# Performance work log

Hardware: AMD Instinct MI355X
Metric: run time of the kernel (lower is better)

## Reference

```python
import jax, jax.numpy as jnp
import numpy as np

N_NODES = 100000
N_EDGES = 1250000
N_GRAPHS = 512
HIDDEN = 64
F_IN = 3
N_CLASSES = 5


def setup_inputs() -> dict:
    key = jax.random.key(0)
    ks = jax.random.split(key, 8)
    x = jax.random.normal(ks[0], (N_NODES, F_IN), dtype=jnp.float32)
    edge_index = jax.random.randint(ks[1], (2, N_EDGES), 0, N_NODES, dtype=jnp.int64)
    batch = jnp.sort(jax.random.randint(ks[2], (N_NODES,), 0, N_GRAPHS, dtype=jnp.int64))
    def glorot(k, shape):
        lim = (6.0 / (shape[0] + shape[1])) ** 0.5
        return jax.random.uniform(k, shape, jnp.float32, -lim, lim)
    return {
        "x": x,
        "edge_index": edge_index,
        "batch": batch,
        "W1": glorot(ks[3], (F_IN, HIDDEN)),
        "b1": jnp.zeros((HIDDEN,), jnp.float32),
        "W2": glorot(ks[4], (HIDDEN, HIDDEN)),
        "b2": jnp.zeros((HIDDEN,), jnp.float32),
        "Wl": glorot(ks[5], (HIDDEN, N_CLASSES)),
        "bl": jnp.zeros((N_CLASSES,), jnp.float32),
    }


def _gcn_conv(x, W, b, src, dst, deg_inv_sqrt):
    # GCNConv: x' = D^{-1/2} (A + I) D^{-1/2} X W + b  (self-loops added)
    h = x @ W                                   # [N, H]
    norm = deg_inv_sqrt[src] * deg_inv_sqrt[dst]  # per-edge scale
    agg = jax.ops.segment_sum(h[src] * norm[:, None], dst, num_segments=N_NODES)
    agg = agg + h * (deg_inv_sqrt * deg_inv_sqrt)[:, None]  # self-loop term
    return agg + b


def reference(x, edge_index, batch, W1, b1, W2, b2, Wl, bl):
    src, dst = edge_index[0], edge_index[1]
    # degree (with self-loop) on destination nodes, as in PyG GCNConv
    ones = jnp.ones((N_EDGES,), jnp.float32)
    deg = jax.ops.segment_sum(ones, dst, num_segments=N_NODES) + 1.0
    deg_inv_sqrt = 1.0 / jnp.sqrt(deg)

    h = jax.nn.relu(_gcn_conv(x, W1, b1, src, dst, deg_inv_sqrt))
    h = _gcn_conv(h, W2, b2, src, dst, deg_inv_sqrt)

    # global_mean_pool over graph ids
    sums = jax.ops.segment_sum(h, batch, num_segments=N_GRAPHS)
    cnts = jax.ops.segment_sum(jnp.ones((N_NODES,), jnp.float32), batch, num_segments=N_GRAPHS)
    pooled = sums / jnp.maximum(cnts, 1.0)[:, None]

    # dropout p=0.5 is identity in eval mode
    return pooled @ Wl + bl
```

## Files before the change

### kernel.cpp

```cpp
#include <hip/hip_runtime.h>
#include <hip/hip_bf16.h>

#define N_NODES   100000
#define N_EDGES   1250000
#define N_GRAPHS  512
#define HIDDEN    64
#define F_IN      3
#define N_CLASSES 5

#define BKT_SHIFT 8
#define BKT_NODES 256
#define N_BKT     ((N_NODES + BKT_NODES - 1) / BKT_NODES)
#define CAP       4096
#define EBLK      512
#define ECHUNK    ((N_EDGES + EBLK - 1) / EBLK)
#define SCT       512
#define NREP      8

__device__ __forceinline__ unsigned short f2bf(float f) {
    unsigned u = __float_as_uint(f);
    u += 0x7FFF + ((u >> 16) & 1);
    return (unsigned short)(u >> 16);
}

__global__ void k_scat(const int* __restrict__ src, const int* __restrict__ dst,
                       const float* __restrict__ W2, const float* __restrict__ Wl,
                       const float* __restrict__ b2, const float* __restrict__ bl,
                       const int* __restrict__ batch,
                       int* __restrict__ gcur, int* __restrict__ ebuf,
                       float* __restrict__ Wc, float* __restrict__ bc,
                       int* __restrict__ gstart) {
    int b = blockIdx.x;
    int tid = threadIdx.x;
    if (b >= EBLK) {
        int bb = b - EBLK;
        if (bb == 0) {
            for (int t = tid; t < HIDDEN * N_CLASSES + N_CLASSES; t += SCT) {
                if (t < HIDDEN * N_CLASSES) {
                    int k = t / N_CLASSES, c = t % N_CLASSES;
                    float acc = 0.0f;
#pragma unroll
                    for (int j = 0; j < HIDDEN; j++)
                        acc = fmaf(W2[k * HIDDEN + j], Wl[j * N_CLASSES + c], acc);
                    Wc[t] = acc;
                } else {
                    int c = t - HIDDEN * N_CLASSES;
                    float acc = bl[c];
#pragma unroll
                    for (int j = 0; j < HIDDEN; j++)
                        acc = fmaf(b2[j], Wl[j * N_CLASSES + c], acc);
                    bc[c] = acc;
                }
            }
            return;
        }
        int n = (bb - 1) * SCT + tid;
        if (n >= N_NODES) return;
        if (n == 0) {
            for (int g = 0; g <= batch[0]; g++) gstart[g] = 0;
        } else {
            int b0 = batch[n - 1], b1 = batch[n];
            for (int g = b0 + 1; g <= b1; g++) gstart[g] = n;
        }
        if (n == N_NODES - 1) {
            for (int g = batch[n] + 1; g <= N_GRAPHS; g++) gstart[g] = N_NODES;
        }
        return;
    }
    __shared__ int pk[ECHUNK];
    __shared__ unsigned short bkl[ECHUNK];
    __shared__ int h[N_BKT];
    __shared__ int cur[N_BKT];
    for (int i = tid; i < N_BKT; i += SCT) h[i] = 0;
    __syncthreads();
    int e0 = b * ECHUNK;
    int m = min(ECHUNK, N_EDGES - e0);
    for (int i = tid; i < m; i += SCT) {
        int s = src[e0 + i], d = dst[e0 + i];
        int bk = d >> BKT_SHIFT;
        pk[i] = (s << BKT_SHIFT) | (d & (BKT_NODES - 1));
        bkl[i] = (unsigned short)bk;
        atomicAdd(&h[bk], 1);
    }
    __syncthreads();
    for (int i = tid; i < N_BKT; i += SCT)
        cur[i] = atomicAdd(&gcur[i], h[i]);
    __syncthreads();
    for (int i = tid; i < m; i += SCT) {
        int bk = bkl[i];
        int lp = atomicAdd(&cur[bk], 1);
        if (lp < CAP)
            ebuf[bk * CAP + lp] = pk[i];
    }
}

__global__ void k_bktfill(const int* __restrict__ ebuf, const int* __restrict__ gcur,
                          const float* __restrict__ x,
                          int* __restrict__ rowptr, int* __restrict__ deg,
                          float* __restrict__ dis, uint2* __restrict__ xs4,
                          int* __restrict__ elist) {
    __shared__ int eb_l[CAP];
    __shared__ int cnt_l[BKT_NODES];
    __shared__ int cur_l[BKT_NODES];
    __shared__ int ps[BKT_NODES];
    int b = blockIdx.x, tid = threadIdx.x;
    int n0 = b * BKT_NODES;
    int e0 = b * CAP;
    int cnt = min(gcur[b], CAP);
    if (tid < BKT_NODES) cnt_l[tid] = 0;
    __syncthreads();
    for (int i = tid; i < cnt; i += 1024) {
        int pe = ebuf[e0 + i];
        eb_l[i] = pe;
        atomicAdd(&cnt_l[pe & (BKT_NODES - 1)], 1);
    }
    __syncthreads();
    if (tid < BKT_NODES) ps[tid] = cnt_l[tid];
    __syncthreads();
    for (int off = 1; off < BKT_NODES; off <<= 1) {
        int t = 0;
        if (tid < BKT_NODES && tid >= off) t = ps[tid - off];
        __syncthreads();
        if (tid < BKT_NODES) ps[tid] += t;
        __syncthreads();
    }
    if (tid < BKT_NODES) {
        int node = n0 + tid;
        int excl = ps[tid] - cnt_l[tid];
        cur_l[tid] = excl;
        if (node < N_NODES) {
            rowptr[node] = e0 + excl;
            deg[node] = cnt_l[tid];
            float dv = rsqrtf((float)cnt_l[tid] + 1.0f);
            dis[node] = dv;
            float x0 = x[node * 3 + 0], x1 = x[node * 3 + 1], x2 = x[node * 3 + 2];
            xs4[node] = make_uint2((unsigned)f2bf(x0 * dv) |
                                   ((unsigned)f2bf(x1 * dv) << 16),
                                   (unsigned)f2bf(x2 * dv));
        }
    }
    __syncthreads();
    for (int i = tid; i < cnt; i += 1024) {
        int pe = eb_l[i];
        int pos = atomicAdd(&cur_l[pe & (BKT_NODES - 1)], 1);
        elist[e0 + pos] = ((unsigned)pe) >> BKT_SHIFT;
    }
}

__global__ void k_l1fused(const int* __restrict__ rp, const int* __restrict__ degA,
                          const int* __restrict__ elist,
                          const float* __restrict__ dis, const uint2* __restrict__ xs4,
                          const float* __restrict__ W1, const float* __restrict__ b1,
                          unsigned* __restrict__ h1b) {
    int w = threadIdx.x >> 6, lane = threadIdx.x & 63;
    int q4 = lane >> 4;
    int j  = lane & 15;
    int node = blockIdx.x * 16 + w * 4 + q4;
    int start = rp[node], dg = degA[node];
    float a0 = 0.f, a1 = 0.f, a2 = 0.f;
    for (int k = 0; k < dg; k += 32) {
        int ia = k + j, ib = k + 16 + j;
        bool aa = ia < dg, ab = ib < dg;
        int sa = elist[start + (aa ? ia : 0)];
        int sb = elist[start + (ab ? ib : 0)];
        uint2 ua = xs4[sa];
        uint2 ub = xs4[sb];
        float ma = aa ? 1.0f : 0.0f;
        float mb = ab ? 1.0f : 0.0f;
        a0 = fmaf(__uint_as_float(ua.x << 16), ma, a0);
        a1 = fmaf(__uint_as_float(ua.x & 0xFFFF0000u), ma, a1);
        a2 = fmaf(__uint_as_float(ua.y << 16), ma, a2);
        a0 = fmaf(__uint_as_float(ub.x << 16), mb, a0);
        a1 = fmaf(__uint_as_float(ub.x & 0xFFFF0000u), mb, a1);
        a2 = fmaf(__uint_as_float(ub.y << 16), mb, a2);
    }
#pragma unroll
    for (int off = 1; off < 16; off <<= 1) {
        a0 += __shfl_xor(a0, off);
        a1 += __shfl_xor(a1, off);
        a2 += __shfl_xor(a2, off);
    }
    uint2 un = xs4[node];
    float dn = dis[node];
    a0 = dn * (a0 + __uint_as_float(un.x << 16));
    a1 = dn * (a1 + __uint_as_float(un.x & 0xFFFF0000u));
    a2 = dn * (a2 + __uint_as_float(un.y << 16));
    float v[4];
#pragma unroll
    for (int i = 0; i < 4; i++) {
        int c = 4 * j + i;
        float t = a0 * W1[c] + a1 * W1[HIDDEN + c] + a2 * W1[2 * HIDDEN + c] + b1[c];
        v[i] = fmaxf(t, 0.0f) * dn;
    }
    unsigned w0 = (unsigned)f2bf(v[0]) | ((unsigned)f2bf(v[1]) << 16);
    unsigned w1 = (unsigned)f2bf(v[2]) | ((unsigned)f2bf(v[3]) << 16);
    *(uint2*)(h1b + (size_t)node * 32 + j * 2) = make_uint2(w0, w1);
}

__global__ void k_gatherpool(const int* __restrict__ rp, const int* __restrict__ degA,
                             const int* __restrict__ elist,
                             const float* __restrict__ dis,
                             const unsigned* __restrict__ h1b,
                             const int* __restrict__ batch,
                             float* __restrict__ gsum8) {
    __shared__ float acc_s[8][HIDDEN];
    __shared__ int gid[8];
    int w = threadIdx.x >> 6, lane = threadIdx.x & 63;
    int half = lane >> 5;
    int l32 = lane & 31;
    int node = blockIdx.x * 8 + w * 2 + half;
    int start = rp[node], dg = degA[node];
    int eg = l32 >> 3;
    int ch = lane & 7;
    float acc[8] = {0.f, 0.f, 0.f, 0.f, 0.f, 0.f, 0.f, 0.f};
    for (int k = 0; k < dg; k += 8) {
        int ia = k + eg;
        int ib = k + 4 + eg;
        bool aa = ia < dg, ab = ib < dg;
        int sa = elist[start + (aa ? ia : 0)];
        int sb = elist[start + (ab ? ib : 0)];
        float ma = aa ? 1.0f : 0.0f;
        float mb = ab ? 1.0f : 0.0f;
        uint4 ua = *(const uint4*)(h1b + (size_t)sa * 32 + ch * 4);
        uint4 ub = *(const uint4*)(h1b + (size_t)sb * 32 + ch * 4);
        acc[0] = fmaf(__uint_as_float(ua.x << 16),          ma, acc[0]);
        acc[1] = fmaf(__uint_as_float(ua.x & 0xFFFF0000u),  ma, acc[1]);
        acc[2] = fmaf(__uint_as_float(ua.y << 16),          ma, acc[2]);
        acc[3] = fmaf(__uint_as_float(ua.y & 0xFFFF0000u),  ma, acc[3]);
        acc[4] = fmaf(__uint_as_float(ua.z << 16),          ma, acc[4]);
        acc[5] = fmaf(__uint_as_float(ua.z & 0xFFFF0000u),  ma, acc[5]);
        acc[6] = fmaf(__uint_as_float(ua.w << 16),          ma, acc[6]);
        acc[7] = fmaf(__uint_as_float(ua.w & 0xFFFF0000u),  ma, acc[7]);
        acc[0] = fmaf(__uint_as_float(ub.x << 16),          mb, acc[0]);
        acc[1] = fmaf(__uint_as_float(ub.x & 0xFFFF0000u),  mb, acc[1]);
        acc[2] = fmaf(__uint_as_float(ub.y << 16),          mb, acc[2]);
        acc[3] = fmaf(__uint_as_float(ub.y & 0xFFFF0000u),  mb, acc[3]);
        acc[4] = fmaf(__uint_as_float(ub.z << 16),          mb, acc[4]);
        acc[5] = fmaf(__uint_as_float(ub.z & 0xFFFF0000u),  mb, acc[5]);
        acc[6] = fmaf(__uint_as_float(ub.w << 16),          mb, acc[6]);
        acc[7] = fmaf(__uint_as_float(ub.w & 0xFFFF0000u),  mb, acc[7]);
    }
#pragma unroll
    for (int i = 0; i < 8; i++) {
        acc[i] += __shfl_xor(acc[i], 8);
        acc[i] += __shfl_xor(acc[i], 16);
    }
    if (l32 == 0) gid[w * 2 + half] = batch[node];
    if (l32 < 8) {
        float dn = dis[node];
        uint4 u = *(const uint4*)(h1b + (size_t)node * 32 + l32 * 4);
        float o[8];
        o[0] = dn * (acc[0] + __uint_as_float(u.x << 16));
        o[1] = dn * (acc[1] + __uint_as_float(u.x & 0xFFFF0000u));
        o[2] = dn * (acc[2] + __uint_as_float(u.y << 16));
        o[3] = dn * (acc[3] + __uint_as_float(u.y & 0xFFFF0000u));
        o[4] = dn * (acc[4] + __uint_as_float(u.z << 16));
        o[5] = dn * (acc[5] + __uint_as_float(u.z & 0xFFFF0000u));
        o[6] = dn * (acc[6] + __uint_as_float(u.w << 16));
        o[7] = dn * (acc[7] + __uint_as_float(u.w & 0xFFFF0000u));
        float* dst = &acc_s[w * 2 + half][l32 * 8];
        *(float4*)(dst)     = make_float4(o[0], o[1], o[2], o[3]);
        *(float4*)(dst + 4) = make_float4(o[4], o[5], o[6], o[7]);
    }
    __syncthreads();
    float* gs = gsum8 + (size_t)(blockIdx.x & (NREP - 1)) * (N_GRAPHS * HIDDEN);
    if (threadIdx.x < HIDDEN) {
        int t = threadIdx.x;
#pragma unroll
        for (int wv = 0; wv < 8; wv++) {
            int gw = gid[wv];
            bool first = true;
#pragma unroll
            for (int u = 0; u < wv; u++)
                if (gid[u] == gw) first = false;
            if (first) {
                float s = acc_s[wv][t];
#pragma unroll
                for (int u2 = wv + 1; u2 < 8; u2++)
                    if (gid[u2] == gw) s += acc_s[u2][t];
                atomicAdd(&gs[gw * HIDDEN + t], s);
            }
        }
    }
}

__global__ void k_head(const float* __restrict__ gsum8, const int* __restrict__ gstart,
                       const float* __restrict__ Wc, const float* __restrict__ bc,
                       float* __restrict__ out) {
    __shared__ float gl[HIDDEN];
    int g = blockIdx.x, t = threadIdx.x;
    float s = 0.0f;
#pragma unroll
    for (int r = 0; r < NREP; r++)
        s += gsum8[(size_t)r * (N_GRAPHS * HIDDEN) + g * HIDDEN + t];
    gl[t] = s;
    __syncthreads();
    if (t < N_CLASSES) {
        float cntf = fmaxf((float)(gstart[g + 1] - gstart[g]), 1.0f);
        float dot = 0.0f;
#pragma unroll
        for (int k = 0; k < HIDDEN; k++)
            dot = fmaf(gl[k], Wc[k * N_CLASSES + t], dot);
        out[g * N_CLASSES + t] = dot / cntf + bc[t];
    }
}

extern "C" void kernel_launch(void* const* d_in, const int* in_sizes, int n_in,
                              void* d_out, int out_size, void* d_ws, size_t ws_size,
                              hipStream_t stream) {
    const float* x     = (const float*)d_in[0];
    const int*   ei    = (const int*)  d_in[1];
    const int*   batch = (const int*)  d_in[2];
    const float* W1    = (const float*)d_in[3];
    const float* b1    = (const float*)d_in[4];
    const float* W2    = (const float*)d_in[5];
    const float* b2    = (const float*)d_in[6];
    const float* Wl    = (const float*)d_in[7];
    const float* bl    = (const float*)d_in[8];
    float* out = (float*)d_out;

    const int* src = ei;
    const int* dst = ei + N_EDGES;

    int*   gcur    = (int*)d_ws;
    float* gsum8   = (float*)(gcur + 512);
    int*   ebuf    = (int*)(gsum8 + NREP * N_GRAPHS * HIDDEN);
    int*   elist   = ebuf + N_BKT * CAP;
    int*   rp      = elist + N_BKT * CAP;
    int*   deg     = rp + N_NODES;
    float* dis     = (float*)(deg + N_NODES);
    uint2* xs4     = (uint2*)(dis + N_NODES);
    unsigned* h1b  = (unsigned*)(xs4 + N_NODES);
    int*   gstart  = (int*)(h1b + (size_t)N_NODES * 32);
    float* Wc      = (float*)(gstart + 516);
    float* bc      = Wc + HIDDEN * N_CLASSES;

    const int BS = 256;
    const int g_nodes_sct = (N_NODES + SCT - 1) / SCT;

    hipMemsetAsync(gcur, 0, (512 + NREP * N_GRAPHS * HIDDEN) * sizeof(int), stream);
    k_scat<<<EBLK + 1 + g_nodes_sct, SCT, 0, stream>>>(src, dst, W2, Wl, b2, bl, batch,
                                                       gcur, ebuf, Wc, bc, gstart);
    k_bktfill<<<N_BKT, 1024, 0, stream>>>(ebuf, gcur, x, rp, deg, dis, xs4, elist);

    k_l1fused<<<N_NODES / 16, BS, 0, stream>>>(rp, deg, elist, dis, xs4, W1, b1,
                                               h1b);

    k_gatherpool<<<N_NODES / 8, BS, 0, stream>>>(rp, deg, elist, dis, h1b,
                                                 batch, gsum8);

    k_head<<<N_GRAPHS, HIDDEN, 0, stream>>>(gsum8, gstart, Wc, bc, out);
}
```

Measured before the change: 154.0 us.

## Stage bucketed edges in LDS for coalesced stores and unroll gather loop

The scatter kernel now runs a local prefix scan over bucket counts and sorts its chunk of edges by bucket in shared memory. It then writes each bucket's run contiguously into the global edge buffer. The bucket-fill kernel likewise builds the per-node sorted edge list in shared memory before a coalesced copy-out. The gather-pool kernel now handles 16 edges per iteration instead of 8, keeping more independent loads in flight. These changes aim to cut scattered global writes and memory latency, at the cost of more shared memory, which may lower occupancy, and extra synchronisations.

```diff
diff --git a/kernel.cpp b/kernel.cpp
--- a/kernel.cpp
+++ b/kernel.cpp
@@ -69,7 +69,11 @@
     }
     __shared__ int pk[ECHUNK];
     __shared__ unsigned short bkl[ECHUNK];
+    __shared__ int spk[ECHUNK];
+    __shared__ unsigned short sbk[ECHUNK];
     __shared__ int h[N_BKT];
+    __shared__ int lsc[N_BKT];
+    __shared__ int gb[N_BKT];
     __shared__ int cur[N_BKT];
     for (int i = tid; i < N_BKT; i += SCT) h[i] = 0;
     __syncthreads();
@@ -83,14 +87,32 @@
         atomicAdd(&h[bk], 1);
     }
     __syncthreads();
-    for (int i = tid; i < N_BKT; i += SCT)
-        cur[i] = atomicAdd(&gcur[i], h[i]);
+    if (tid < N_BKT) lsc[tid] = h[tid];
+    __syncthreads();
+    for (int off = 1; off < N_BKT; off <<= 1) {
+        int t = 0;
+        if (tid < N_BKT && tid >= off) t = lsc[tid - off];
+        __syncthreads();
+        if (tid < N_BKT) lsc[tid] += t;
+        __syncthreads();
+    }
+    if (tid < N_BKT) {
+        gb[tid] = atomicAdd(&gcur[tid], h[tid]);
+        cur[tid] = lsc[tid] - h[tid];
+    }
     __syncthreads();
     for (int i = tid; i < m; i += SCT) {
         int bk = bkl[i];
-        int lp = atomicAdd(&cur[bk], 1);
-        if (lp < CAP)
-            ebuf[bk * CAP + lp] = pk[i];
+        int p = atomicAdd(&cur[bk], 1);
+        spk[p] = pk[i];
+        sbk[p] = (unsigned short)bk;
+    }
+    __syncthreads();
+    for (int i = tid; i < m; i += SCT) {
+        int bk = sbk[i];
+        int gpos = gb[bk] + (i - (lsc[bk] - h[bk]));
+        if (gpos < CAP)
+            ebuf[bk * CAP + gpos] = spk[i];
     }
 }
 
@@ -100,6 +122,7 @@
                           float* __restrict__ dis, uint2* __restrict__ xs4,
                           int* __restrict__ elist) {
     __shared__ int eb_l[CAP];
+    __shared__ int sorted_l[CAP];
     __shared__ int cnt_l[BKT_NODES];
     __shared__ int cur_l[BKT_NODES];
     __shared__ int ps[BKT_NODES];
@@ -143,8 +166,11 @@
     for (int i = tid; i < cnt; i += 1024) {
         int pe = eb_l[i];
         int pos = atomicAdd(&cur_l[pe & (BKT_NODES - 1)], 1);
-        elist[e0 + pos] = ((unsigned)pe) >> BKT_SHIFT;
-    }
+        sorted_l[pos] = ((unsigned)pe) >> BKT_SHIFT;
+    }
+    __syncthreads();
+    for (int i = tid; i < cnt; i += 1024)
+        elist[e0 + i] = sorted_l[i];
 }
 
 __global__ void k_l1fused(const int* __restrict__ rp, const int* __restrict__ degA,
@@ -213,32 +239,53 @@
     int eg = l32 >> 3;
     int ch = lane & 7;
     float acc[8] = {0.f, 0.f, 0.f, 0.f, 0.f, 0.f, 0.f, 0.f};
-    for (int k = 0; k < dg; k += 8) {
-        int ia = k + eg;
-        int ib = k + 4 + eg;
-        bool aa = ia < dg, ab = ib < dg;
-        int sa = elist[start + (aa ? ia : 0)];
-        int sb = elist[start + (ab ? ib : 0)];
-        float ma = aa ? 1.0f : 0.0f;
-        float mb = ab ? 1.0f : 0.0f;
-        uint4 ua = *(const uint4*)(h1b + (size_t)sa * 32 + ch * 4);
-        uint4 ub = *(const uint4*)(h1b + (size_t)sb * 32 + ch * 4);
-        acc[0] = fmaf(__uint_as_float(ua.x << 16),          ma, acc[0]);
-        acc[1] = fmaf(__uint_as_float(ua.x & 0xFFFF0000u),  ma, acc[1]);
-        acc[2] = fmaf(__uint_as_float(ua.y << 16),          ma, acc[2]);
-        acc[3] = fmaf(__uint_as_float(ua.y & 0xFFFF0000u),  ma, acc[3]);
-        acc[4] = fmaf(__uint_as_float(ua.z << 16),          ma, acc[4]);
-        acc[5] = fmaf(__uint_as_float(ua.z & 0xFFFF0000u),  ma, acc[5]);
-        acc[6] = fmaf(__uint_as_float(ua.w << 16),          ma, acc[6]);
-        acc[7] = fmaf(__uint_as_float(ua.w & 0xFFFF0000u),  ma, acc[7]);
-        acc[0] = fmaf(__uint_as_float(ub.x << 16),          mb, acc[0]);
-        acc[1] = fmaf(__uint_as_float(ub.x & 0xFFFF0000u),  mb, acc[1]);
-        acc[2] = fmaf(__uint_as_float(ub.y << 16),          mb, acc[2]);
-        acc[3] = fmaf(__uint_as_float(ub.y & 0xFFFF0000u),  mb, acc[3]);
-        acc[4] = fmaf(__uint_as_float(ub.z << 16),          mb, acc[4]);
-        acc[5] = fmaf(__uint_as_float(ub.z & 0xFFFF0000u),  mb, acc[5]);
-        acc[6] = fmaf(__uint_as_float(ub.w << 16),          mb, acc[6]);
-        acc[7] = fmaf(__uint_as_float(ub.w & 0xFFFF0000u),  mb, acc[7]);
+    for (int k = 0; k < dg; k += 16) {
+        int i0 = k + eg, i1 = k + 4 + eg, i2 = k + 8 + eg, i3 = k + 12 + eg;
+        bool a0b = i0 < dg, a1b = i1 < dg, a2b = i2 < dg, a3b = i3 < dg;
+        int s0 = elist[start + (a0b ? i0 : 0)];
+        int s1 = elist[start + (a1b ? i1 : 0)];
+        int s2 = elist[start + (a2b ? i2 : 0)];
+        int s3 = elist[start + (a3b ? i3 : 0)];
+        float m0 = a0b ? 1.0f : 0.0f;
+        float m1 = a1b ? 1.0f : 0.0f;
+        float m2 = a2b ? 1.0f : 0.0f;
+        float m3 = a3b ? 1.0f : 0.0f;
+        uint4 u0 = *(const uint4*)(h1b + (size_t)s0 * 32 + ch * 4);
+        uint4 u1 = *(const uint4*)(h1b + (size_t)s1 * 32 + ch * 4);
+        uint4 u2 = *(const uint4*)(h1b + (size_t)s2 * 32 + ch * 4);
+        uint4 u3 = *(const uint4*)(h1b + (size_t)s3 * 32 + ch * 4);
+        acc[0] = fmaf(__uint_as_float(u0.x << 16),          m0, acc[0]);
+        acc[1] = fmaf(__uint_as_float(u0.x & 0xFFFF0000u),  m0, acc[1]);
+        acc[2] = fmaf(__uint_as_float(u0.y << 16),          m0, acc[2]);
+        acc[3] = fmaf(__uint_as_float(u0.y & 0xFFFF0000u),  m0, acc[3]);
+        acc[4] = fmaf(__uint_as_float(u0.z << 16),          m0, acc[4]);
+        acc[5] = fmaf(__uint_as_float(u0.z & 0xFFFF0000u),  m0, acc[5]);
+        acc[6] = fmaf(__uint_as_float(u0.w << 16),          m0, acc[6]);
+        acc[7] = fmaf(__uint_as_float(u0.w & 0xFFFF0000u),  m0, acc[7]);
+        acc[0] = fmaf(__uint_as_float(u1.x << 16),          m1, acc[0]);
+        acc[1] = fmaf(__uint_as_float(u1.x & 0xFFFF0000u),  m1, acc[1]);
+        acc[2] = fmaf(__uint_as_float(u1.y << 16),          m1, acc[2]);
+        acc[3] = fmaf(__uint_as_float(u1.y & 0xFFFF0000u),  m1, acc[3]);
+        acc[4] = fmaf(__uint_as_float(u1.z << 16),          m1, acc[4]);
+        acc[5] = fmaf(__uint_as_float(u1.z & 0xFFFF0000u),  m1, acc[5]);
+        acc[6] = fmaf(__uint_as_float(u1.w << 16),          m1, acc[6]);
+        acc[7] = fmaf(__uint_as_float(u1.w & 0xFFFF0000u),  m1, acc[7]);
+        acc[0] = fmaf(__uint_as_float(u2.x << 16),          m2, acc[0]);
+        acc[1] = fmaf(__uint_as_float(u2.x & 0xFFFF0000u),  m2, acc[1]);
+        acc[2] = fmaf(__uint_as_float(u2.y << 16),          m2, acc[2]);
+        acc[3] = fmaf(__uint_as_float(u2.y & 0xFFFF0000u),  m2, acc[3]);
+        acc[4] = fmaf(__uint_as_float(u2.z << 16),          m2, acc[4]);
+        acc[5] = fmaf(__uint_as_float(u2.z & 0xFFFF0000u),  m2, acc[5]);
+        acc[6] = fmaf(__uint_as_float(u2.w << 16),          m2, acc[6]);
+        acc[7] = fmaf(__uint_as_float(u2.w & 0xFFFF0000u),  m2, acc[7]);
+        acc[0] = fmaf(__uint_as_float(u3.x << 16),          m3, acc[0]);
+        acc[1] = fmaf(__uint_as_float(u3.x & 0xFFFF0000u),  m3, acc[1]);
+        acc[2] = fmaf(__uint_as_float(u3.y << 16),          m3, acc[2]);
+        acc[3] = fmaf(__uint_as_float(u3.y & 0xFFFF0000u),  m3, acc[3]);
+        acc[4] = fmaf(__uint_as_float(u3.z << 16),          m3, acc[4]);
+        acc[5] = fmaf(__uint_as_float(u3.z & 0xFFFF0000u),  m3, acc[5]);
+        acc[6] = fmaf(__uint_as_float(u3.w << 16),          m3, acc[6]);
+        acc[7] = fmaf(__uint_as_float(u3.w & 0xFFFF0000u),  m3, acc[7]);
     }
 #pragma unroll
     for (int i = 0; i < 8; i++) {
```

After: 143.8 us. 6.6% less time.
